# Kernel optimization log

Measured on AMD Instinct MI355X. Metric: run time of the kernel, lower is better.

## Reference

```python
import jax, jax.numpy as jnp
import numpy as np

N, D, K = 262144, 64, 1024


def setup_inputs() -> dict:
    key = jax.random.key(0)
    kx, kc = jax.random.split(key)
    x = jax.random.normal(kx, (N, D), dtype=jnp.float32)
    codebook = jax.random.normal(kc, (K, D), dtype=jnp.float32)
    return {"x": x, "codebook": codebook}


def reference(x, codebook):
    # VQTokenizer.encode: cdist(x, codebook) -> argmin -> gather.
    # squared distances equals argmin over cdist (sqrt is monotone).
    x2 = jnp.sum(x * x, axis=-1, keepdims=True)            # (N, 1)
    c2 = jnp.sum(codebook * codebook, axis=-1)             # (K,)
    d2 = x2 + c2[None, :] - 2.0 * jnp.einsum('nd,kd->nk', x, codebook)  # (N, K)
    encoded = jnp.argmin(d2, axis=1)                       # (N,) int
    quantized = jnp.take(codebook, encoded, axis=0)        # (N, D)
    return encoded, quantized
```

## Files before the change

### kernel.cpp

```cpp
#include <hip/hip_runtime.h>
#include <hip/hip_bf16.h>

#define NPTS 262144
#define DDIM 64
#define KCB  1024
#define CHUNK 128
#define NCHUNK (KCB / CHUNK)
#define GPC (CHUNK / 16)
#define PPB 256

typedef __attribute__((ext_vector_type(8))) short short8;
typedef __attribute__((ext_vector_type(4))) float f32x4;

static __device__ __forceinline__ unsigned short f2bf_rne(float f) {
    union { float f; unsigned u; } v; v.f = f;
    unsigned r = v.u + 0x7FFFu + ((v.u >> 16) & 1u);
    return (unsigned short)(r >> 16);
}
static __device__ __forceinline__ float bf2f(unsigned short h) {
    union { unsigned u; float f; } v; v.u = ((unsigned)h) << 16;
    return v.f;
}
static __device__ __forceinline__ bool beats(float sa, int ka, float sb, int kb) {
    return (sa > sb) || (sa == sb && ka < kb);
}
static __device__ __forceinline__ float keyf(float acc, unsigned inv) {
    return __uint_as_float((__float_as_uint(acc) & 0xFFFFFFC0u) | inv);
}

__global__ __launch_bounds__(256) void c2n_kernel(const float* __restrict__ cb,
                                                  float* __restrict__ c2n) {
    int k = blockIdx.x * blockDim.x + threadIdx.x;
    if (k >= KCB) return;
    const float4* row = (const float4*)(cb + (size_t)k * DDIM);
    float s0 = 0.f, s1 = 0.f, s2 = 0.f, s3 = 0.f;
#pragma unroll
    for (int j = 0; j < DDIM / 4; ++j) {
        float4 a = row[j];
        s0 = __builtin_fmaf(a.x, a.x, s0);
        s1 = __builtin_fmaf(a.y, a.y, s1);
        s2 = __builtin_fmaf(a.z, a.z, s2);
        s3 = __builtin_fmaf(a.w, a.w, s3);
    }
    c2n[k] = 256.0f - 0.5f * ((s0 + s1) + (s2 + s3));
}

__global__ __launch_bounds__(256) void pack_kernel(const float* __restrict__ cb,
                                                   unsigned short* __restrict__ G) {
    int t = blockIdx.x * 256 + threadIdx.x;
    int r = t >> 3, d8 = t & 7;
    const float4* src = (const float4*)(cb + (size_t)r * DDIM + d8 * 8);
    float4 v0 = src[0], v1 = src[1];
    float vv[8] = {v0.x, v0.y, v0.z, v0.w, v1.x, v1.y, v1.z, v1.w};
    short8 h, l;
#pragma unroll
    for (int j = 0; j < 8; ++j) {
        unsigned short hb = f2bf_rne(vv[j]);
        h[j] = (short)hb;
        l[j] = (short)f2bf_rne(vv[j] - bf2f(hb));
    }
    int c = r >> 7, g = (r >> 4) & 7, col = r & 15;
    int ks = d8 >> 2, q = d8 & 3;
    size_t base = (size_t)c * 16384 + g * 1024 + ks * 512 + q * 128 + col * 8;
    *(short8*)(G + base) = h;
    *(short8*)(G + base + 8192) = l;
}

struct BFrag { short8 h0, l0, h1, l1; };

__global__ __launch_bounds__(512, 4) void vq_main(const float* __restrict__ x,
                                                  const float* __restrict__ cb,
                                                  const float* __restrict__ c2n,
                                                  const unsigned short* __restrict__ G,
                                                  float* __restrict__ out) {
    __shared__ unsigned short frag[2][CHUNK * DDIM * 2];
    __shared__ float lds_c2f[KCB];
    __shared__ int lds_bk1[PPB];
    __shared__ int lds_bk2[PPB];

    const int tid = threadIdx.x;
    const int lane = tid & 63;
    const int wave = tid >> 6;
    const int b15 = lane & 15;
    const int q = lane >> 4;
    const int blk_base = blockIdx.x * PPB;
    const int wave_base = blk_base + wave * 32;
    const int lane_off = lane * 16;

    short8 Ahi[2][2], Alo[2][2];
#pragma unroll
    for (int t = 0; t < 2; ++t) {
        const float* xr = x + (size_t)(wave_base + t * 16 + b15) * DDIM + q * 8;
#pragma unroll
        for (int ks = 0; ks < 2; ++ks) {
            float4 v0 = *(const float4*)(xr + ks * 32);
            float4 v1 = *(const float4*)(xr + ks * 32 + 4);
            float vv[8] = {v0.x, v0.y, v0.z, v0.w, v1.x, v1.y, v1.z, v1.w};
            short8 h, l;
#pragma unroll
            for (int j = 0; j < 8; ++j) {
                unsigned short hb = f2bf_rne(vv[j]);
                h[j] = (short)hb;
                l[j] = (short)f2bf_rne(vv[j] - bf2f(hb));
            }
            Ahi[t][ks] = h;
            Alo[t][ks] = l;
        }
    }

    float b1[8], b2[8];
#pragma unroll
    for (int i = 0; i < 8; ++i) { b1[i] = 0.0f; b2[i] = 0.0f; }

#define STAGE(cc, buf)                                                                     \
    {                                                                                      \
        const unsigned char* gsrc = (const unsigned char*)G + (size_t)(cc) * 32768 + tid * 16; \
        unsigned char* ldst = (unsigned char*)&frag[buf][0] + tid * 16;                    \
        _Pragma("unroll") for (int it = 0; it < 4; ++it)                                   \
            __builtin_amdgcn_global_load_lds(                                              \
                (const __attribute__((address_space(1))) unsigned int*)(gsrc + it * 8192), \
                (__attribute__((address_space(3))) unsigned int*)(ldst + it * 8192),       \
                16, 0, 0);                                                                 \
    }
#define LOADB(dst, fb, g)                                               \
    {                                                                   \
        const unsigned char* p_ = (fb) + (size_t)(g) * 2048 + lane_off; \
        (dst).h0 = *(const short8*)(p_);                                \
        (dst).l0 = *(const short8*)(p_ + 16384);                        \
        (dst).h1 = *(const short8*)(p_ + 1024);                         \
        (dst).l1 = *(const short8*)(p_ + 17408);                        \
    }
#define COMPUTE(acc, B, cvec)                                                                    \
    {                                                                                            \
        __builtin_amdgcn_s_setprio(1);                                                           \
        _Pragma("unroll") for (int t = 0; t < 2; ++t) {                                          \
            acc[t] = __builtin_amdgcn_mfma_f32_16x16x32_bf16(Ahi[t][0], (B).h0, cvec, 0, 0, 0);  \
            acc[t] = __builtin_amdgcn_mfma_f32_16x16x32_bf16(Ahi[t][0], (B).l0, acc[t], 0, 0, 0);\
            acc[t] = __builtin_amdgcn_mfma_f32_16x16x32_bf16(Alo[t][0], (B).h0, acc[t], 0, 0, 0);\
            acc[t] = __builtin_amdgcn_mfma_f32_16x16x32_bf16(Ahi[t][1], (B).h1, acc[t], 0, 0, 0);\
            acc[t] = __builtin_amdgcn_mfma_f32_16x16x32_bf16(Ahi[t][1], (B).l1, acc[t], 0, 0, 0);\
            acc[t] = __builtin_amdgcn_mfma_f32_16x16x32_bf16(Alo[t][1], (B).h1, acc[t], 0, 0, 0);\
        }                                                                                        \
        __builtin_amdgcn_s_setprio(0);                                                           \
    }

    STAGE(0, 0);
    lds_c2f[tid] = c2n[tid];
    lds_c2f[tid + 512] = c2n[tid + 512];
    __syncthreads();

    for (int cc = 0; cc < NCHUNK; ++cc) {
        const int cur = cc & 1;
        if (cc + 1 < NCHUNK) STAGE(cc + 1, cur ^ 1);
        const unsigned char* fb = (const unsigned char*)&frag[cur][0];

#pragma unroll
        for (int j = 0; j < 4; ++j) {
            const int ga = (wave + 2 * j) & 7;
            const int gb = (ga + 1) & 7;
            const unsigned inva = 63u - (unsigned)(cc * GPC + ga);
            const unsigned invb = 63u - (unsigned)(cc * GPC + gb);
            BFrag Ba, Bb;
            LOADB(Ba, fb, ga);
            LOADB(Bb, fb, gb);
            const float cga = lds_c2f[(cc * GPC + ga) * 16 + b15];
            const float cgb = lds_c2f[(cc * GPC + gb) * 16 + b15];

            f32x4 acc0[2];
            const f32x4 cvec0 = (f32x4){cga, cga, cga, cga};
            COMPUTE(acc0, Ba, cvec0);
            f32x4 acc1[2];
            const f32x4 cvec1 = (f32x4){cgb, cgb, cgb, cgb};
            COMPUTE(acc1, Bb, cvec1);

#pragma unroll
            for (int t = 0; t < 2; ++t)
#pragma unroll
                for (int r = 0; r < 4; ++r) {
                    const int i = t * 4 + r;
                    const float ka = keyf(acc0[t][r], inva);
                    const float kb = keyf(acc1[t][r], invb);
                    const float med = __builtin_amdgcn_fmed3f(b1[i], ka, kb);
                    float nb1;
                    asm("v_max3_f32 %0, %1, %2, %3"
                        : "=v"(nb1) : "v"(b1[i]), "v"(ka), "v"(kb));
                    b1[i] = nb1;
                    b2[i] = fmaxf(b2[i], med);
                }
        }
        __syncthreads();
    }
#undef STAGE
#undef LOADB
#undef COMPUTE

    unsigned int K1[8], K2[8];
    int I1[8], I2[8];
#pragma unroll
    for (int i = 0; i < 8; ++i) {
        K1[i] = __float_as_uint(b1[i]); I1[i] = (int)(63u - (K1[i] & 63u)) * 16 + b15;
        K2[i] = __float_as_uint(b2[i]); I2[i] = (int)(63u - (K2[i] & 63u)) * 16 + b15;
    }
#pragma unroll
    for (int m = 1; m < 16; m <<= 1) {
#pragma unroll
        for (int i = 0; i < 8; ++i) {
            unsigned int o1 = __shfl_xor(K1[i], m); int oi1 = __shfl_xor(I1[i], m);
            unsigned int o2 = __shfl_xor(K2[i], m); int oi2 = __shfl_xor(I2[i], m);
            bool ob = (o1 > K1[i]) || (o1 == K1[i] && oi1 < I1[i]);
            unsigned int nk1, nk2; int ni1, ni2;
            if (ob) {
                nk1 = o1; ni1 = oi1;
                bool sb = (K1[i] > o2) || (K1[i] == o2 && I1[i] < oi2);
                nk2 = sb ? K1[i] : o2; ni2 = sb ? I1[i] : oi2;
            } else {
                nk1 = K1[i]; ni1 = I1[i];
                bool sb = (o1 > K2[i]) || (o1 == K2[i] && oi1 < I2[i]);
                nk2 = sb ? o1 : K2[i]; ni2 = sb ? oi1 : I2[i];
            }
            K1[i] = nk1; I1[i] = ni1; K2[i] = nk2; I2[i] = ni2;
        }
    }

    if (b15 == 0) {
#pragma unroll
        for (int t = 0; t < 2; ++t)
#pragma unroll
            for (int r = 0; r < 4; ++r) {
                int pl = wave * 32 + t * 16 + q * 4 + r;
                lds_bk1[pl] = I1[t * 4 + r];
                lds_bk2[pl] = I2[t * 4 + r];
            }
    }
    __syncthreads();

    const int pid = tid >> 1;
    const int p = blk_base + pid;
    const int ksel = (tid & 1) ? lds_bk2[pid] : lds_bk1[pid];
    const float4* xr = (const float4*)(x + (size_t)p * DDIM);
    const float4* cr = (const float4*)(cb + (size_t)ksel * DDIM);
    float da = 0.f, db = 0.f;
#pragma unroll
    for (int j = 0; j < 16; ++j) {
        float4 xv = xr[j];
        float4 u = cr[j];
        da = __builtin_fmaf(xv.x, u.x, da); db = __builtin_fmaf(xv.y, u.y, db);
        da = __builtin_fmaf(xv.z, u.z, da); db = __builtin_fmaf(xv.w, u.w, db);
    }
    float a = (da + db) + lds_c2f[ksel];
    float oa = __shfl_xor(a, 1);
    int ok = __shfl_xor(ksel, 1);
    const bool first = ((tid & 1) == 0);
    float a1 = first ? a : oa; int k1 = first ? ksel : ok;
    float a2 = first ? oa : a; int k2 = first ? ok : ksel;
    int kf = beats(a1, k1, a2, k2) ? k1 : k2;

    if (first) out[p] = (float)kf;
    const float4* cf = (const float4*)(cb + (size_t)kf * DDIM + (tid & 1) * 32);
    float4* qo = (float4*)(out + NPTS + (size_t)p * DDIM + (tid & 1) * 32);
#pragma unroll
    for (int j = 0; j < 8; ++j) qo[j] = cf[j];
}

extern "C" void kernel_launch(void* const* d_in, const int* in_sizes, int n_in,
                              void* d_out, int out_size, void* d_ws, size_t ws_size,
                              hipStream_t stream) {
    const float* x = (const float*)d_in[0];
    const float* cb = (const float*)d_in[1];
    float* c2n = (float*)d_ws;
    unsigned short* G = (unsigned short*)((char*)d_ws + 4096);

    hipLaunchKernelGGL(c2n_kernel, dim3(KCB / 256), dim3(256), 0, stream, cb, c2n);
    hipLaunchKernelGGL(pack_kernel, dim3(KCB * 8 / 256), dim3(256), 0, stream, cb, G);
    hipLaunchKernelGGL(vq_main, dim3(NPTS / PPB), dim3(512), 0, stream,
                       x, cb, c2n, G, (float*)d_out);
}
```

Measured before the change: 148.9 us.

## Fuse codebook prep kernels, drop setprio, hoist centroid norms and unstagger groups

Merges the codebook norm and bf16 hi/lo packing kernels into one prep kernel, which computes the norm with a lane shuffle reduction, saving one launch. In the main kernel the s_setprio hints around the MFMA blocks are removed. The per-group c2 values are now loaded once per chunk into registers, and every wave walks the groups in the same fixed order instead of a wave-staggered order. The fixed order may raise LDS bank conflicts, since all waves now read the same fragments at once, and it adds register pressure for the cached norms.

After: 135.2 us. -9.2%, faster.

```diff
diff --git a/kernel.cpp b/kernel.cpp
--- a/kernel.cpp
+++ b/kernel.cpp
@@ -28,42 +28,32 @@
     return __uint_as_float((__float_as_uint(acc) & 0xFFFFFFC0u) | inv);
 }
 
-__global__ __launch_bounds__(256) void c2n_kernel(const float* __restrict__ cb,
-                                                  float* __restrict__ c2n) {
-    int k = blockIdx.x * blockDim.x + threadIdx.x;
-    if (k >= KCB) return;
-    const float4* row = (const float4*)(cb + (size_t)k * DDIM);
-    float s0 = 0.f, s1 = 0.f, s2 = 0.f, s3 = 0.f;
-#pragma unroll
-    for (int j = 0; j < DDIM / 4; ++j) {
-        float4 a = row[j];
-        s0 = __builtin_fmaf(a.x, a.x, s0);
-        s1 = __builtin_fmaf(a.y, a.y, s1);
-        s2 = __builtin_fmaf(a.z, a.z, s2);
-        s3 = __builtin_fmaf(a.w, a.w, s3);
-    }
-    c2n[k] = 256.0f - 0.5f * ((s0 + s1) + (s2 + s3));
-}
-
-__global__ __launch_bounds__(256) void pack_kernel(const float* __restrict__ cb,
-                                                   unsigned short* __restrict__ G) {
+__global__ __launch_bounds__(256) void prep_kernel(const float* __restrict__ cb,
+                                                   unsigned short* __restrict__ G,
+                                                   float* __restrict__ c2n) {
     int t = blockIdx.x * 256 + threadIdx.x;
     int r = t >> 3, d8 = t & 7;
     const float4* src = (const float4*)(cb + (size_t)r * DDIM + d8 * 8);
     float4 v0 = src[0], v1 = src[1];
     float vv[8] = {v0.x, v0.y, v0.z, v0.w, v1.x, v1.y, v1.z, v1.w};
     short8 h, l;
+    float s = 0.f;
 #pragma unroll
     for (int j = 0; j < 8; ++j) {
         unsigned short hb = f2bf_rne(vv[j]);
         h[j] = (short)hb;
         l[j] = (short)f2bf_rne(vv[j] - bf2f(hb));
+        s = __builtin_fmaf(vv[j], vv[j], s);
     }
     int c = r >> 7, g = (r >> 4) & 7, col = r & 15;
     int ks = d8 >> 2, q = d8 & 3;
     size_t base = (size_t)c * 16384 + g * 1024 + ks * 512 + q * 128 + col * 8;
     *(short8*)(G + base) = h;
     *(short8*)(G + base + 8192) = l;
+    s += __shfl_xor(s, 1);
+    s += __shfl_xor(s, 2);
+    s += __shfl_xor(s, 4);
+    if (d8 == 0) c2n[r] = 256.0f - 0.5f * s;
 }
 
 struct BFrag { short8 h0, l0, h1, l1; };
@@ -132,7 +122,6 @@
     }
 #define COMPUTE(acc, B, cvec)                                                                    \
     {                                                                                            \
-        __builtin_amdgcn_s_setprio(1);                                                           \
         _Pragma("unroll") for (int t = 0; t < 2; ++t) {                                          \
             acc[t] = __builtin_amdgcn_mfma_f32_16x16x32_bf16(Ahi[t][0], (B).h0, cvec, 0, 0, 0);  \
             acc[t] = __builtin_amdgcn_mfma_f32_16x16x32_bf16(Ahi[t][0], (B).l0, acc[t], 0, 0, 0);\
@@ -141,7 +130,6 @@
             acc[t] = __builtin_amdgcn_mfma_f32_16x16x32_bf16(Ahi[t][1], (B).l1, acc[t], 0, 0, 0);\
             acc[t] = __builtin_amdgcn_mfma_f32_16x16x32_bf16(Alo[t][1], (B).h1, acc[t], 0, 0, 0);\
         }                                                                                        \
-        __builtin_amdgcn_s_setprio(0);                                                           \
     }
 
     STAGE(0, 0);
@@ -154,23 +142,23 @@
         if (cc + 1 < NCHUNK) STAGE(cc + 1, cur ^ 1);
         const unsigned char* fb = (const unsigned char*)&frag[cur][0];
 
+        float cg[GPC];
+#pragma unroll
+        for (int g = 0; g < GPC; ++g) cg[g] = lds_c2f[(cc * GPC + g) * 16 + b15];
+
 #pragma unroll
         for (int j = 0; j < 4; ++j) {
-            const int ga = (wave + 2 * j) & 7;
-            const int gb = (ga + 1) & 7;
-            const unsigned inva = 63u - (unsigned)(cc * GPC + ga);
-            const unsigned invb = 63u - (unsigned)(cc * GPC + gb);
+            const int g0 = 2 * j, g1 = 2 * j + 1;
+            const unsigned inv0 = 63u - (unsigned)(cc * GPC + g0);
             BFrag Ba, Bb;
-            LOADB(Ba, fb, ga);
-            LOADB(Bb, fb, gb);
-            const float cga = lds_c2f[(cc * GPC + ga) * 16 + b15];
-            const float cgb = lds_c2f[(cc * GPC + gb) * 16 + b15];
+            LOADB(Ba, fb, g0);
+            LOADB(Bb, fb, g1);
 
             f32x4 acc0[2];
-            const f32x4 cvec0 = (f32x4){cga, cga, cga, cga};
+            const f32x4 cvec0 = (f32x4){cg[g0], cg[g0], cg[g0], cg[g0]};
             COMPUTE(acc0, Ba, cvec0);
             f32x4 acc1[2];
-            const f32x4 cvec1 = (f32x4){cgb, cgb, cgb, cgb};
+            const f32x4 cvec1 = (f32x4){cg[g1], cg[g1], cg[g1], cg[g1]};
             COMPUTE(acc1, Bb, cvec1);
 
 #pragma unroll
@@ -178,8 +166,8 @@
 #pragma unroll
                 for (int r = 0; r < 4; ++r) {
                     const int i = t * 4 + r;
-                    const float ka = keyf(acc0[t][r], inva);
-                    const float kb = keyf(acc1[t][r], invb);
+                    const float ka = keyf(acc0[t][r], inv0);
+                    const float kb = keyf(acc1[t][r], inv0 - 1u);
                     const float med = __builtin_amdgcn_fmed3f(b1[i], ka, kb);
                     float nb1;
                     asm("v_max3_f32 %0, %1, %2, %3"
@@ -270,8 +258,7 @@
     float* c2n = (float*)d_ws;
     unsigned short* G = (unsigned short*)((char*)d_ws + 4096);
 
-    hipLaunchKernelGGL(c2n_kernel, dim3(KCB / 256), dim3(256), 0, stream, cb, c2n);
-    hipLaunchKernelGGL(pack_kernel, dim3(KCB * 8 / 256), dim3(256), 0, stream, cb, G);
+    hipLaunchKernelGGL(prep_kernel, dim3(KCB * 8 / 256), dim3(256), 0, stream, cb, G, c2n);
     hipLaunchKernelGGL(vq_main, dim3(NPTS / PPB), dim3(512), 0, stream,
                        x, cb, c2n, G, (float*)d_out);
 }
```
